# Kernel tuning notes

Measured on AMD Instinct MI355X. Metric: run time of the kernel, lower is better.

Reference implementation:

```python
import jax, jax.numpy as jnp
import numpy as np

N = 100000   # nodes
P = 3        # metapaths
E = 800000   # edges per metapath (avg degree 8)
IN = 128     # in_size
H = 4        # layer_num_heads
D = 32       # out_size per head
HID = 64     # semantic attention hidden
NEG_SLOPE = 0.2


def setup_inputs() -> dict:
    key = jax.random.key(0)
    ks = jax.random.split(key, 10)
    h = jax.random.normal(ks[0], (N, IN), jnp.float32)
    edge_src = jax.random.randint(ks[1], (P, E), 0, N, dtype=jnp.int32).astype(jnp.int64)
    edge_dst = jax.random.randint(ks[2], (P, E), 0, N, dtype=jnp.int32).astype(jnp.int64)
    W = jax.random.normal(ks[3], (P, IN, H * D), jnp.float32) * 0.05
    attn_l = jax.random.normal(ks[4], (P, H, D), jnp.float32) * 0.05
    attn_r = jax.random.normal(ks[5], (P, H, D), jnp.float32) * 0.05
    bias = jnp.zeros((P, H * D), jnp.float32)
    sa_w1 = jax.random.normal(ks[6], (H * D, HID), jnp.float32) * 0.05
    sa_b1 = jnp.zeros((HID,), jnp.float32)
    sa_w2 = jax.random.normal(ks[7], (HID, 1), jnp.float32) * 0.05
    return {"h": h, "edge_src": edge_src, "edge_dst": edge_dst, "W": W,
            "attn_l": attn_l, "attn_r": attn_r, "bias": bias,
            "sa_w1": sa_w1, "sa_b1": sa_b1, "sa_w2": sa_w2}


def _gat_conv(h, src, dst, Wp, al, ar, bp):
    # DGL GATConv: project, per-edge additive attention, edge softmax over dst, scatter-sum.
    n = h.shape[0]
    feat = (h @ Wp).reshape(n, H, D)              # [N,H,D]
    el = (feat * al).sum(-1)                      # [N,H]
    er = (feat * ar).sum(-1)                      # [N,H]
    e = jax.nn.leaky_relu(el[src] + er[dst], NEG_SLOPE)   # [E,H]
    emax = jax.ops.segment_max(e, dst, num_segments=n)    # [N,H]
    emax = jnp.where(jnp.isfinite(emax), emax, 0.0)       # zero-in-degree guard
    ex = jnp.exp(e - emax[dst])                            # [E,H]
    denom = jax.ops.segment_sum(ex, dst, num_segments=n)   # [N,H]
    alpha = ex / jnp.maximum(denom[dst], 1e-9)              # [E,H]
    msg = alpha[:, :, None] * feat[src]                     # [E,H,D]
    out = jax.ops.segment_sum(msg, dst, num_segments=n)     # [N,H,D]
    return out.reshape(n, H * D) + bp


def reference(h, edge_src, edge_dst, W, attn_l, attn_r, bias, sa_w1, sa_b1, sa_w2):
    embs = []
    for p in range(P):  # small fixed metapath set
        embs.append(_gat_conv(h, edge_src[p], edge_dst[p], W[p], attn_l[p], attn_r[p], bias[p]))
    z = jnp.stack(embs, axis=1)                 # [N,P,H*D]
    # SemanticAttention: MLP score, mean over nodes, softmax over metapaths
    w = (jnp.tanh(z @ sa_w1 + sa_b1) @ sa_w2).mean(0)   # [P,1]
    beta = jax.nn.softmax(w, axis=0)                     # [P,1]
    return (beta[None, :, :] * z).sum(1)                 # [N,H*D]
```

## Files before the change

kernel.cpp:

```cpp
#include <hip/hip_runtime.h>
#include <hip/hip_bf16.h>
#include <math.h>

#define NN 100000
#define NP 3
#define NE 800000
#define NH 4
#define ND 32
#define HD 128
#define NHID 64
#define CAP 48

#define S64 64
#define SLICEW 1568
#define CAPB 13504
#define EPT 16
#define FCHUNK (256 * EPT)

typedef __attribute__((ext_vector_type(8))) short short8;
typedef __attribute__((ext_vector_type(4))) float f32x4;

__device__ __forceinline__ unsigned short f2bf(float f) {
  union { float f; unsigned int u; } v; v.f = f;
  unsigned int r = v.u + 0x7FFFu + ((v.u >> 16) & 1u);
  return (unsigned short)(r >> 16);
}
__device__ __forceinline__ float bf2f(unsigned short u) {
  return __uint_as_float(((unsigned int)u) << 16);
}
__device__ __forceinline__ float tanh_fast(float x) {
  return 1.f - 2.f / (1.f + __expf(2.f * x));
}

__global__ __launch_bounds__(256) void prep_kernel(
    const float* __restrict__ h, const float* __restrict__ W, const float* __restrict__ W1,
    unsigned short* __restrict__ hb, unsigned short* __restrict__ WT,
    unsigned short* __restrict__ W1T, int* __restrict__ bucketCnt, float* __restrict__ s) {
  int i = blockIdx.x * blockDim.x + threadIdx.x;
  if (i < NN * 32) {
    float4 v = ((const float4*)h)[i];
    ushort4 o;
    o.x = f2bf(v.x); o.y = f2bf(v.y); o.z = f2bf(v.z); o.w = f2bf(v.w);
    ((ushort4*)hb)[i] = o;
  }
  if (i < NP * 128 * 128) {
    int p = i >> 14, r = i & 16383, n = r >> 7, k = r & 127;
    WT[i] = f2bf(W[(size_t)p * 16384 + k * 128 + n]);
  }
  if (i < NHID * 128) {
    int n = i >> 7, k = i & 127;
    W1T[i] = f2bf(W1[(size_t)k * NHID + n]);
  }
  if (i < NP * S64) bucketCnt[i] = 0;
  if (i < 4) s[i] = 0.f;
}

__global__ __launch_bounds__(256) void gemm_mfma_kernel(
    const unsigned short* __restrict__ hb, const unsigned short* __restrict__ WT_all,
    const float* __restrict__ al_all, const float* __restrict__ ar_all,
    unsigned short* __restrict__ featb_all, float* __restrict__ el_all,
    float* __restrict__ er_all) {
  __shared__ unsigned short Bs[128 * 128];
  const int p = blockIdx.y;
  const unsigned short* WTp = WT_all + (size_t)p * 16384;
#pragma unroll
  for (int it = 0; it < 8; ++it)
    ((float4*)Bs)[it * 256 + threadIdx.x] = ((const float4*)WTp)[it * 256 + threadIdx.x];
  __syncthreads();

  const int wid = threadIdx.x >> 6, lane = threadIdx.x & 63;
  const int c = lane & 15, q = lane >> 4;
  const int tile = blockIdx.x * 4 + wid;
  const int tc = tile < 6250 ? tile : 6249;

  f32x4 acc[8];
#pragma unroll
  for (int t = 0; t < 8; ++t) acc[t] = (f32x4){0.f, 0.f, 0.f, 0.f};

  const unsigned short* arow = hb + (size_t)(tc * 16 + c) * 128 + q * 8;
#pragma unroll
  for (int kc = 0; kc < 4; ++kc) {
    short8 a = *(const short8*)(arow + kc * 32);
#pragma unroll
    for (int t = 0; t < 8; ++t) {
      short8 b = *(const short8*)(Bs + (size_t)(t * 16 + c) * 128 + kc * 32 + q * 8);
      acc[t] = __builtin_amdgcn_mfma_f32_16x16x32_bf16(a, b, acc[t], 0, 0, 0);
    }
  }
  if (tile >= 6250) return;

  unsigned short* featb = featb_all + (size_t)p * NN * 128;
#pragma unroll
  for (int t = 0; t < 8; ++t)
#pragma unroll
    for (int i = 0; i < 4; ++i)
      featb[(size_t)(tc * 16 + q * 4 + i) * 128 + t * 16 + c] = f2bf(acc[t][i]);

  const float* al = al_all + p * 128;
  const float* ar = ar_all + p * 128;
  float alv[8], arv[8];
#pragma unroll
  for (int t = 0; t < 8; ++t) { alv[t] = al[t * 16 + c]; arv[t] = ar[t * 16 + c]; }
  float elp[4][4], erp[4][4];
#pragma unroll
  for (int i = 0; i < 4; ++i)
#pragma unroll
    for (int hh = 0; hh < 4; ++hh) {
      elp[i][hh] = acc[2 * hh][i] * alv[2 * hh] + acc[2 * hh + 1][i] * alv[2 * hh + 1];
      erp[i][hh] = acc[2 * hh][i] * arv[2 * hh] + acc[2 * hh + 1][i] * arv[2 * hh + 1];
    }
#pragma unroll
  for (int m = 1; m <= 8; m <<= 1)
#pragma unroll
    for (int i = 0; i < 4; ++i)
#pragma unroll
      for (int hh = 0; hh < 4; ++hh) {
        elp[i][hh] += __shfl_xor(elp[i][hh], m);
        erp[i][hh] += __shfl_xor(erp[i][hh], m);
      }
  if (c == 0) {
    float* el = el_all + (size_t)p * NN * 4;
    float* er = er_all + (size_t)p * NN * 4;
#pragma unroll
    for (int i = 0; i < 4; ++i) {
      int row = tc * 16 + q * 4 + i;
      *(float4*)(el + (size_t)row * 4) = make_float4(elp[i][0], elp[i][1], elp[i][2], elp[i][3]);
      *(float4*)(er + (size_t)row * 4) = make_float4(erp[i][0], erp[i][1], erp[i][2], erp[i][3]);
    }
  }
}

__global__ __launch_bounds__(256) void fillA_kernel(
    const int* __restrict__ src_all, const int* __restrict__ dst_all,
    int* __restrict__ bucketCnt, int* __restrict__ pairs) {
  __shared__ int histA[S64];
  __shared__ int baseA[S64];
  const int p = blockIdx.y;
  const int e0 = blockIdx.x * FCHUNK + threadIdx.x;
  const int* dstp = dst_all + (size_t)p * NE;
  const int* srcp = src_all + (size_t)p * NE;
  if (threadIdx.x < S64) histA[threadIdx.x] = 0;
  __syncthreads();
  int dv[EPT], sv[EPT];
#pragma unroll
  for (int k = 0; k < EPT; ++k) {
    int e = e0 + k * 256;
    dv[k] = -1; sv[k] = 0;
    if (e < NE) {
      dv[k] = __builtin_nontemporal_load(dstp + e);
      sv[k] = __builtin_nontemporal_load(srcp + e);
    }
    if (dv[k] >= 0) atomicAdd(&histA[(unsigned)dv[k] / SLICEW], 1);
  }
  __syncthreads();
  if (threadIdx.x < S64) {
    baseA[threadIdx.x] = atomicAdd(&bucketCnt[p * S64 + threadIdx.x], histA[threadIdx.x]);
    histA[threadIdx.x] = 0;
  }
  __syncthreads();
#pragma unroll
  for (int k = 0; k < EPT; ++k) {
    if (dv[k] >= 0) {
      int sl = (unsigned)dv[k] / SLICEW;
      int pos = baseA[sl] + atomicAdd(&histA[sl], 1);
      if (pos < CAPB) {
        int dl = dv[k] - sl * SLICEW;
        pairs[((size_t)p * S64 + sl) * CAPB + pos] = (dl << 17) | sv[k];
      }
    }
  }
}

__global__ __launch_bounds__(1024) void fillB_kernel(
    const int* __restrict__ bucketCnt, const int* __restrict__ pairs,
    int* __restrict__ cnt_all, int* __restrict__ elist_all) {
  __shared__ int hist[SLICEW];
  const int p = blockIdx.y, sl = blockIdx.x;
  for (int i = threadIdx.x; i < SLICEW; i += 1024) hist[i] = 0;
  __syncthreads();
  int total = bucketCnt[p * S64 + sl];
  if (total > CAPB) total = CAPB;
  const int* pr = pairs + ((size_t)p * S64 + sl) * CAPB;
  int* elp = elist_all + (size_t)p * NN * CAP;
  for (int i = threadIdx.x; i < total; i += 1024) {
    int pk = pr[i];
    int src = pk & 0x1FFFF;
    int dl = pk >> 17;
    int pos = atomicAdd(&hist[dl], 1);
    if (pos < CAP) elp[(size_t)(sl * SLICEW + dl) * CAP + pos] = src;
  }
  __syncthreads();
  int* cntp = cnt_all + (size_t)p * NN;
  for (int i = threadIdx.x; i < SLICEW; i += 1024) {
    int n = sl * SLICEW + i;
    if (n < NN) cntp[n] = hist[i];
  }
}

__global__ __launch_bounds__(256) void gather_kernel(
    const unsigned short* __restrict__ featb_all, const float* __restrict__ el_all,
    const float* __restrict__ er_all, const int* __restrict__ cnt_all,
    const int* __restrict__ elist_all, const float* __restrict__ bias_all,
    unsigned short* __restrict__ zb) {
  const int p = blockIdx.y;
  const unsigned short* featb = featb_all + (size_t)p * NN * 128;
  const float* el = el_all + (size_t)p * NN * 4;
  const int* elist = elist_all + (size_t)p * NN * CAP;
  const int wid = threadIdx.x >> 6;
  const int lane = threadIdx.x & 63;
  const int n = blockIdx.x * 4 + wid;
  int deg = cnt_all[(size_t)p * NN + n]; deg = deg > CAP ? CAP : deg;
  float4 ern = *(const float4*)(er_all + (size_t)p * NN * 4 + (size_t)n * 4);

  const int j16 = lane & 15, hgrp = lane >> 4;
  const float ernh = hgrp == 0 ? ern.x : hgrp == 1 ? ern.y : hgrp == 2 ? ern.z : ern.w;
  const int sub = lane >> 4, c16 = lane & 15;
  const int hh = c16 >> 2;

  float acc[8] = {0.f, 0.f, 0.f, 0.f, 0.f, 0.f, 0.f, 0.f};
  float dsum = 0.f;

  for (int b = 0; b < deg; b += 16) {
    int s = 0; float x = 0.f;
    int jj = b + j16;
    if (jj < deg) {
      s = elist[(size_t)n * CAP + jj];
      float ev = el[(size_t)s * 4 + hgrp];
      float e = ev + ernh; e = fmaxf(e, 0.2f * e);
      x = __expf(e);
    }
    int bend = deg - b; bend = bend > 16 ? 16 : bend;
    for (int i = 0; i < bend; i += 8) {
      int j0 = i + sub, j1 = i + 4 + sub;
      int s0 = __shfl(s, j0);
      int s1 = __shfl(s, j1);
      float xv0 = __shfl(x, (hh << 4) | j0);
      float xv1 = __shfl(x, (hh << 4) | j1);
      short8 f0 = *(const short8*)(featb + (size_t)s0 * 128 + c16 * 8);
      short8 f1 = *(const short8*)(featb + (size_t)s1 * 128 + c16 * 8);
      dsum += xv0 + xv1;
#pragma unroll
      for (int k = 0; k < 8; ++k) acc[k] += xv0 * bf2f((unsigned short)f0[k]);
#pragma unroll
      for (int k = 0; k < 8; ++k) acc[k] += xv1 * bf2f((unsigned short)f1[k]);
    }
  }
  dsum += __shfl_xor(dsum, 16); dsum += __shfl_xor(dsum, 32);
#pragma unroll
  for (int k = 0; k < 8; ++k) {
    acc[k] += __shfl_xor(acc[k], 16);
    acc[k] += __shfl_xor(acc[k], 32);
  }
  if (sub == 0) {
    float rd = dsum > 0.f ? 1.f / dsum : 0.f;
    const float* bias = bias_all + p * 128 + c16 * 8;
    float4 b0 = *(const float4*)(bias);
    float4 b1 = *(const float4*)(bias + 4);
    short8 o;
    o[0] = f2bf(acc[0] * rd + b0.x); o[1] = f2bf(acc[1] * rd + b0.y);
    o[2] = f2bf(acc[2] * rd + b0.z); o[3] = f2bf(acc[3] * rd + b0.w);
    o[4] = f2bf(acc[4] * rd + b1.x); o[5] = f2bf(acc[5] * rd + b1.y);
    o[6] = f2bf(acc[6] * rd + b1.z); o[7] = f2bf(acc[7] * rd + b1.w);
    *(short8*)(zb + (size_t)n * (NP * 128) + p * 128 + c16 * 8) = o;
  }
}

__global__ __launch_bounds__(256) void sem_mfma_kernel(
    const unsigned short* __restrict__ zb, const unsigned short* __restrict__ W1T,
    const float* __restrict__ b1, const float* __restrict__ w2,
    float* __restrict__ s) {
  __shared__ float red3[3];
  if (threadIdx.x < 3) red3[threadIdx.x] = 0.f;
  __syncthreads();
  const int wid = threadIdx.x >> 6, lane = threadIdx.x & 63;
  const int tile = blockIdx.x * 4 + wid;
  const bool active = tile < 18750;
  const int tc = active ? tile : 18749;
  const int c = lane & 15, q = lane >> 4;
  f32x4 acc[4];
#pragma unroll
  for (int t = 0; t < 4; ++t) acc[t] = (f32x4){0.f, 0.f, 0.f, 0.f};

  const unsigned short* arow = zb + (size_t)(tc * 16 + c) * 128 + q * 8;
  const unsigned short* brow = W1T + (size_t)c * 128 + q * 8;
#pragma unroll
  for (int kc = 0; kc < 4; ++kc) {
    short8 a = *(const short8*)(arow + kc * 32);
#pragma unroll
    for (int t = 0; t < 4; ++t) {
      short8 b = *(const short8*)(brow + (size_t)t * 16 * 128 + kc * 32);
      acc[t] = __builtin_amdgcn_mfma_f32_16x16x32_bf16(a, b, acc[t], 0, 0, 0);
    }
  }
  float part[4] = {0.f, 0.f, 0.f, 0.f};
#pragma unroll
  for (int t = 0; t < 4; ++t) {
    float bb = b1[t * 16 + c], ww = w2[t * 16 + c];
#pragma unroll
    for (int i = 0; i < 4; ++i) part[i] += tanh_fast(acc[t][i] + bb) * ww;
  }
#pragma unroll
  for (int m = 1; m <= 8; m <<= 1)
#pragma unroll
    for (int i = 0; i < 4; ++i) part[i] += __shfl_xor(part[i], m);
  if (active && c == 0) {
#pragma unroll
    for (int i = 0; i < 4; ++i)
      atomicAdd(&red3[(tc * 16 + q * 4 + i) % 3], part[i]);
  }
  __syncthreads();
  if (threadIdx.x < 3) atomicAdd(&s[threadIdx.x], red3[threadIdx.x]);
}

__global__ __launch_bounds__(256) void final_kernel(
    const unsigned short* __restrict__ zb, const float* __restrict__ s,
    float* __restrict__ out) {
  int i = blockIdx.x * blockDim.x + threadIdx.x;
  if (i >= NN * 16) return;
  float w0 = s[0] * (1.f / NN), w1 = s[1] * (1.f / NN), w2c = s[2] * (1.f / NN);
  float m = fmaxf(w0, fmaxf(w1, w2c));
  float e0 = __expf(w0 - m), e1 = __expf(w1 - m), e2 = __expf(w2c - m);
  float inv = 1.f / (e0 + e1 + e2);
  float b0 = e0 * inv, b1 = e1 * inv, b2 = e2 * inv;
  int n = i >> 4, g = i & 15;
  const unsigned short* zr = zb + (size_t)n * (NP * 128) + g * 8;
  ushort4 u0a = *(const ushort4*)(zr);
  ushort4 u0b = *(const ushort4*)(zr + 4);
  ushort4 u1a = *(const ushort4*)(zr + 128);
  ushort4 u1b = *(const ushort4*)(zr + 132);
  ushort4 u2a = *(const ushort4*)(zr + 256);
  ushort4 u2b = *(const ushort4*)(zr + 260);
  float4 oa, ob;
  oa.x = b0 * bf2f(u0a.x) + b1 * bf2f(u1a.x) + b2 * bf2f(u2a.x);
  oa.y = b0 * bf2f(u0a.y) + b1 * bf2f(u1a.y) + b2 * bf2f(u2a.y);
  oa.z = b0 * bf2f(u0a.z) + b1 * bf2f(u1a.z) + b2 * bf2f(u2a.z);
  oa.w = b0 * bf2f(u0a.w) + b1 * bf2f(u1a.w) + b2 * bf2f(u2a.w);
  ob.x = b0 * bf2f(u0b.x) + b1 * bf2f(u1b.x) + b2 * bf2f(u2b.x);
  ob.y = b0 * bf2f(u0b.y) + b1 * bf2f(u1b.y) + b2 * bf2f(u2b.y);
  ob.z = b0 * bf2f(u0b.z) + b1 * bf2f(u1b.z) + b2 * bf2f(u2b.z);
  ob.w = b0 * bf2f(u0b.w) + b1 * bf2f(u1b.w) + b2 * bf2f(u2b.w);
  float* op = out + (size_t)n * 128 + g * 8;
  *(float4*)op = oa;
  *(float4*)(op + 4) = ob;
}

extern "C" void kernel_launch(void* const* d_in, const int* in_sizes, int n_in,
                              void* d_out, int out_size, void* d_ws, size_t ws_size,
                              hipStream_t stream) {
  const float* h    = (const float*)d_in[0];
  const int*   esrc = (const int*)d_in[1];
  const int*   edst = (const int*)d_in[2];
  const float* W    = (const float*)d_in[3];
  const float* al   = (const float*)d_in[4];
  const float* ar   = (const float*)d_in[5];
  const float* bias = (const float*)d_in[6];
  const float* w1   = (const float*)d_in[7];
  const float* b1   = (const float*)d_in[8];
  const float* w2   = (const float*)d_in[9];
  float* out = (float*)d_out;

  unsigned short* zb    = (unsigned short*)d_ws;
  int* pairs = (int*)d_ws;
  unsigned short* featb = zb + (size_t)38400000;
  unsigned short* WT    = featb + (size_t)38400000;
  unsigned short* W1T   = WT + 49152;
  float* el   = (float*)(W1T + 8192);
  float* er   = el + (size_t)NP * NN * 4;
  float* s    = er + (size_t)NP * NN * 4;
  float* beta = s + 16;
  int* bucketCnt = (int*)(beta + 16);
  int* cnt   = bucketCnt + 256;
  int* elist = cnt + (size_t)NP * NN;
  unsigned short* hb = (unsigned short*)elist;

  prep_kernel<<<(NN * 32 + 255) / 256, 256, 0, stream>>>(h, W, w1, hb, WT, W1T, bucketCnt, s);

  dim3 gemmGrid(NN / 64 + 1, NP);
  gemm_mfma_kernel<<<gemmGrid, 256, 0, stream>>>(hb, WT, al, ar, featb, el, er);

  dim3 fillAGrid((NE + FCHUNK - 1) / FCHUNK, NP);
  fillA_kernel<<<fillAGrid, 256, 0, stream>>>(esrc, edst, bucketCnt, pairs);

  dim3 fillBGrid(S64, NP);
  fillB_kernel<<<fillBGrid, 1024, 0, stream>>>(bucketCnt, pairs, cnt, elist);

  dim3 gatherGrid(NN / 4, NP);
  gather_kernel<<<gatherGrid, 256, 0, stream>>>(featb, el, er, cnt, elist, bias, zb);

  sem_mfma_kernel<<<(18750 + 3) / 4, 256, 0, stream>>>(zb, W1T, b1, w2, s);
  final_kernel<<<(NN * 16 + 255) / 256, 256, 0, stream>>>(zb, s, out);
}
```

Baseline: 461.6 us.

## Fuse edge bucketing into prep and CSR build into a slice-local gather kernel

Edge bucketing no longer runs as a separate fillA launch. It moves into the prep kernel and writes per-block histograms and local offsets into fixed per-chunk regions, so no global atomics are needed. The fillB and gather kernels are merged into one gather2 kernel. Each block owns 256 destination nodes, collects their edges from all chunks with a binary search over a prefix scan, sorts them in LDS, and then runs the same attention aggregation. This removes two launches and the padded per-node edge list round trip through global memory, at the cost of serial scans in LDS and far fewer, heavier gather blocks (391×3 of 512 threads). Edges beyond 2560 per slice are dropped.

```diff
diff --git a/kernel.cpp b/kernel.cpp
--- a/kernel.cpp
+++ b/kernel.cpp
@@ -9,13 +9,14 @@
 #define ND 32
 #define HD 128
 #define NHID 64
-#define CAP 48
-
-#define S64 64
-#define SLICEW 1568
-#define CAPB 13504
+
+#define SLW 256
+#define SBK 512
+#define GB 391
+#define NBLK 196
+#define ECHUNK 4096
 #define EPT 16
-#define FCHUNK (256 * EPT)
+#define EMAX 2560
 
 typedef __attribute__((ext_vector_type(8))) short short8;
 typedef __attribute__((ext_vector_type(4))) float f32x4;
@@ -32,27 +33,81 @@
   return 1.f - 2.f / (1.f + __expf(2.f * x));
 }
 
-__global__ __launch_bounds__(256) void prep_kernel(
+__global__ __launch_bounds__(256) void prep_fill_kernel(
     const float* __restrict__ h, const float* __restrict__ W, const float* __restrict__ W1,
+    const int* __restrict__ src_all, const int* __restrict__ dst_all,
     unsigned short* __restrict__ hb, unsigned short* __restrict__ WT,
-    unsigned short* __restrict__ W1T, int* __restrict__ bucketCnt, float* __restrict__ s) {
-  int i = blockIdx.x * blockDim.x + threadIdx.x;
-  if (i < NN * 32) {
-    float4 v = ((const float4*)h)[i];
-    ushort4 o;
-    o.x = f2bf(v.x); o.y = f2bf(v.y); o.z = f2bf(v.z); o.w = f2bf(v.w);
-    ((ushort4*)hb)[i] = o;
-  }
-  if (i < NP * 128 * 128) {
-    int p = i >> 14, r = i & 16383, n = r >> 7, k = r & 127;
-    WT[i] = f2bf(W[(size_t)p * 16384 + k * 128 + n]);
-  }
-  if (i < NHID * 128) {
-    int n = i >> 7, k = i & 127;
-    W1T[i] = f2bf(W1[(size_t)k * NHID + n]);
-  }
-  if (i < NP * S64) bucketCnt[i] = 0;
-  if (i < 4) s[i] = 0.f;
+    unsigned short* __restrict__ W1T, float* __restrict__ s,
+    int* __restrict__ cntA, int* __restrict__ baseA, int* __restrict__ pairs) {
+  __shared__ int hist[SBK];
+  __shared__ int scanb[SBK];
+  const int tid = threadIdx.x;
+  const int bx = blockIdx.x;
+  if (bx < 12500) {
+    int i = bx * 256 + tid;
+    if (i < NN * 32) {
+      float4 v = ((const float4*)h)[i];
+      ushort4 o;
+      o.x = f2bf(v.x); o.y = f2bf(v.y); o.z = f2bf(v.z); o.w = f2bf(v.w);
+      ((ushort4*)hb)[i] = o;
+    }
+    if (i < NP * 128 * 128) {
+      int p = i >> 14, r = i & 16383, n = r >> 7, k = r & 127;
+      WT[i] = f2bf(W[(size_t)p * 16384 + k * 128 + n]);
+    }
+    if (i < NHID * 128) {
+      int n = i >> 7, k = i & 127;
+      W1T[i] = f2bf(W1[(size_t)k * NHID + n]);
+    }
+    if (i < 4) s[i] = 0.f;
+    return;
+  }
+  const int b2 = bx - 12500;
+  const int p = b2 / NBLK, blk = b2 % NBLK;
+  const int* dstp = dst_all + (size_t)p * NE;
+  const int* srcp = src_all + (size_t)p * NE;
+  hist[tid] = 0; hist[tid + 256] = 0;
+  __syncthreads();
+  int dv[EPT], sv[EPT];
+#pragma unroll
+  for (int k = 0; k < EPT; ++k) {
+    int e = blk * ECHUNK + k * 256 + tid;
+    dv[k] = -1; sv[k] = 0;
+    if (e < NE) {
+      dv[k] = __builtin_nontemporal_load(dstp + e);
+      sv[k] = __builtin_nontemporal_load(srcp + e);
+    }
+    if (dv[k] >= 0) atomicAdd(&hist[(unsigned)dv[k] >> 8], 1);
+  }
+  __syncthreads();
+  scanb[tid] = hist[tid]; scanb[tid + 256] = hist[tid + 256];
+  __syncthreads();
+  for (int off = 1; off < SBK; off <<= 1) {
+    int a0 = (tid >= off) ? scanb[tid - off] : 0;
+    int a1 = scanb[tid + 256 - off];
+    __syncthreads();
+    scanb[tid] += a0; scanb[tid + 256] += a1;
+    __syncthreads();
+  }
+  int c0 = hist[tid], c1 = hist[tid + 256];
+  int b0 = scanb[tid] - c0, b1 = scanb[tid + 256] - c1;
+  int* cA = cntA + ((size_t)p * NBLK + blk) * SBK;
+  int* bA = baseA + ((size_t)p * NBLK + blk) * SBK;
+  cA[tid] = c0; cA[tid + 256] = c1;
+  bA[tid] = b0; bA[tid + 256] = b1;
+  __syncthreads();
+  scanb[tid] = b0; scanb[tid + 256] = b1;
+  hist[tid] = 0; hist[tid + 256] = 0;
+  __syncthreads();
+  int* prp = pairs + (size_t)p * NE + (size_t)blk * ECHUNK;
+#pragma unroll
+  for (int k = 0; k < EPT; ++k) {
+    if (dv[k] >= 0) {
+      int sl = (unsigned)dv[k] >> 8;
+      int pos = scanb[sl] + atomicAdd(&hist[sl], 1);
+      prp[pos] = ((dv[k] & 255) << 17) | sv[k];
+    }
+  }
 }
 
 __global__ __launch_bounds__(256) void gemm_mfma_kernel(
@@ -130,138 +185,127 @@
   }
 }
 
-__global__ __launch_bounds__(256) void fillA_kernel(
-    const int* __restrict__ src_all, const int* __restrict__ dst_all,
-    int* __restrict__ bucketCnt, int* __restrict__ pairs) {
-  __shared__ int histA[S64];
-  __shared__ int baseA[S64];
-  const int p = blockIdx.y;
-  const int e0 = blockIdx.x * FCHUNK + threadIdx.x;
-  const int* dstp = dst_all + (size_t)p * NE;
-  const int* srcp = src_all + (size_t)p * NE;
-  if (threadIdx.x < S64) histA[threadIdx.x] = 0;
-  __syncthreads();
-  int dv[EPT], sv[EPT];
-#pragma unroll
-  for (int k = 0; k < EPT; ++k) {
-    int e = e0 + k * 256;
-    dv[k] = -1; sv[k] = 0;
-    if (e < NE) {
-      dv[k] = __builtin_nontemporal_load(dstp + e);
-      sv[k] = __builtin_nontemporal_load(srcp + e);
-    }
-    if (dv[k] >= 0) atomicAdd(&histA[(unsigned)dv[k] / SLICEW], 1);
-  }
-  __syncthreads();
-  if (threadIdx.x < S64) {
-    baseA[threadIdx.x] = atomicAdd(&bucketCnt[p * S64 + threadIdx.x], histA[threadIdx.x]);
-    histA[threadIdx.x] = 0;
-  }
-  __syncthreads();
-#pragma unroll
-  for (int k = 0; k < EPT; ++k) {
-    if (dv[k] >= 0) {
-      int sl = (unsigned)dv[k] / SLICEW;
-      int pos = baseA[sl] + atomicAdd(&histA[sl], 1);
-      if (pos < CAPB) {
-        int dl = dv[k] - sl * SLICEW;
-        pairs[((size_t)p * S64 + sl) * CAPB + pos] = (dl << 17) | sv[k];
-      }
-    }
-  }
-}
-
-__global__ __launch_bounds__(1024) void fillB_kernel(
-    const int* __restrict__ bucketCnt, const int* __restrict__ pairs,
-    int* __restrict__ cnt_all, int* __restrict__ elist_all) {
-  __shared__ int hist[SLICEW];
+__global__ __launch_bounds__(512) void gather2_kernel(
+    const unsigned short* __restrict__ featb_all, const float* __restrict__ el_all,
+    const float* __restrict__ er_all, const int* __restrict__ cntA,
+    const int* __restrict__ baseA, const int* __restrict__ pairs,
+    const float* __restrict__ bias_all, unsigned short* __restrict__ zb) {
+  __shared__ int scnt[NBLK];
+  __shared__ int sbase[NBLK];
+  __shared__ int scum[NBLK];
+  __shared__ int totE;
+  __shared__ int hist[SLW];
+  __shared__ int start[SLW];
+  __shared__ int wcur[SLW];
+  __shared__ int earr[EMAX];
+  __shared__ int srt[EMAX];
+  const int tid = threadIdx.x;
   const int p = blockIdx.y, sl = blockIdx.x;
-  for (int i = threadIdx.x; i < SLICEW; i += 1024) hist[i] = 0;
-  __syncthreads();
-  int total = bucketCnt[p * S64 + sl];
-  if (total > CAPB) total = CAPB;
-  const int* pr = pairs + ((size_t)p * S64 + sl) * CAPB;
-  int* elp = elist_all + (size_t)p * NN * CAP;
-  for (int i = threadIdx.x; i < total; i += 1024) {
-    int pk = pr[i];
-    int src = pk & 0x1FFFF;
-    int dl = pk >> 17;
-    int pos = atomicAdd(&hist[dl], 1);
-    if (pos < CAP) elp[(size_t)(sl * SLICEW + dl) * CAP + pos] = src;
-  }
-  __syncthreads();
-  int* cntp = cnt_all + (size_t)p * NN;
-  for (int i = threadIdx.x; i < SLICEW; i += 1024) {
-    int n = sl * SLICEW + i;
-    if (n < NN) cntp[n] = hist[i];
-  }
-}
-
-__global__ __launch_bounds__(256) void gather_kernel(
-    const unsigned short* __restrict__ featb_all, const float* __restrict__ el_all,
-    const float* __restrict__ er_all, const int* __restrict__ cnt_all,
-    const int* __restrict__ elist_all, const float* __restrict__ bias_all,
-    unsigned short* __restrict__ zb) {
-  const int p = blockIdx.y;
+
+  for (int b = tid; b < NBLK; b += 512) {
+    scnt[b] = cntA[((size_t)p * NBLK + b) * SBK + sl];
+    sbase[b] = baseA[((size_t)p * NBLK + b) * SBK + sl];
+  }
+  if (tid < SLW) hist[tid] = 0;
+  __syncthreads();
+  if (tid < NBLK) scum[tid] = scnt[tid];
+  __syncthreads();
+  for (int off = 1; off < NBLK; off <<= 1) {
+    int a = (tid < NBLK && tid >= off) ? scum[tid - off] : 0;
+    __syncthreads();
+    if (tid < NBLK) scum[tid] += a;
+    __syncthreads();
+  }
+  if (tid == NBLK - 1) { int t = scum[NBLK - 1]; totE = t > EMAX ? EMAX : t; }
+  int excl = (tid < NBLK) ? scum[tid] - scnt[tid] : 0;
+  __syncthreads();
+  if (tid < NBLK) scum[tid] = excl;
+  __syncthreads();
+  const int total = totE;
+  const int* prp = pairs + (size_t)p * NE;
+  for (int e = tid; e < total; e += 512) {
+    int lo = 0, hi = NBLK - 1;
+    while (lo < hi) { int mid = (lo + hi + 1) >> 1; if (scum[mid] <= e) lo = mid; else hi = mid - 1; }
+    int pk = prp[(size_t)lo * ECHUNK + sbase[lo] + (e - scum[lo])];
+    earr[e] = pk;
+    atomicAdd(&hist[pk >> 17], 1);
+  }
+  __syncthreads();
+  if (tid < SLW) start[tid] = hist[tid];
+  __syncthreads();
+  for (int off = 1; off < SLW; off <<= 1) {
+    int a = (tid < SLW && tid >= off) ? start[tid - off] : 0;
+    __syncthreads();
+    if (tid < SLW) start[tid] += a;
+    __syncthreads();
+  }
+  if (tid < SLW) { int st = start[tid] - hist[tid]; start[tid] = st; wcur[tid] = st; }
+  __syncthreads();
+  for (int e = tid; e < total; e += 512) {
+    int pk = earr[e];
+    int pos = atomicAdd(&wcur[pk >> 17], 1);
+    srt[pos] = pk & 0x1FFFF;
+  }
+  __syncthreads();
+
   const unsigned short* featb = featb_all + (size_t)p * NN * 128;
   const float* el = el_all + (size_t)p * NN * 4;
-  const int* elist = elist_all + (size_t)p * NN * CAP;
-  const int wid = threadIdx.x >> 6;
-  const int lane = threadIdx.x & 63;
-  const int n = blockIdx.x * 4 + wid;
-  int deg = cnt_all[(size_t)p * NN + n]; deg = deg > CAP ? CAP : deg;
-  float4 ern = *(const float4*)(er_all + (size_t)p * NN * 4 + (size_t)n * 4);
-
+  const int w = tid >> 6, lane = tid & 63;
   const int j16 = lane & 15, hgrp = lane >> 4;
-  const float ernh = hgrp == 0 ? ern.x : hgrp == 1 ? ern.y : hgrp == 2 ? ern.z : ern.w;
   const int sub = lane >> 4, c16 = lane & 15;
   const int hh = c16 >> 2;
-
-  float acc[8] = {0.f, 0.f, 0.f, 0.f, 0.f, 0.f, 0.f, 0.f};
-  float dsum = 0.f;
-
-  for (int b = 0; b < deg; b += 16) {
-    int s = 0; float x = 0.f;
-    int jj = b + j16;
-    if (jj < deg) {
-      s = elist[(size_t)n * CAP + jj];
-      float ev = el[(size_t)s * 4 + hgrp];
-      float e = ev + ernh; e = fmaxf(e, 0.2f * e);
-      x = __expf(e);
-    }
-    int bend = deg - b; bend = bend > 16 ? 16 : bend;
-    for (int i = 0; i < bend; i += 8) {
-      int j0 = i + sub, j1 = i + 4 + sub;
-      int s0 = __shfl(s, j0);
-      int s1 = __shfl(s, j1);
-      float xv0 = __shfl(x, (hh << 4) | j0);
-      float xv1 = __shfl(x, (hh << 4) | j1);
-      short8 f0 = *(const short8*)(featb + (size_t)s0 * 128 + c16 * 8);
-      short8 f1 = *(const short8*)(featb + (size_t)s1 * 128 + c16 * 8);
-      dsum += xv0 + xv1;
-#pragma unroll
-      for (int k = 0; k < 8; ++k) acc[k] += xv0 * bf2f((unsigned short)f0[k]);
-#pragma unroll
-      for (int k = 0; k < 8; ++k) acc[k] += xv1 * bf2f((unsigned short)f1[k]);
-    }
-  }
-  dsum += __shfl_xor(dsum, 16); dsum += __shfl_xor(dsum, 32);
-#pragma unroll
-  for (int k = 0; k < 8; ++k) {
-    acc[k] += __shfl_xor(acc[k], 16);
-    acc[k] += __shfl_xor(acc[k], 32);
-  }
-  if (sub == 0) {
-    float rd = dsum > 0.f ? 1.f / dsum : 0.f;
-    const float* bias = bias_all + p * 128 + c16 * 8;
-    float4 b0 = *(const float4*)(bias);
-    float4 b1 = *(const float4*)(bias + 4);
-    short8 o;
-    o[0] = f2bf(acc[0] * rd + b0.x); o[1] = f2bf(acc[1] * rd + b0.y);
-    o[2] = f2bf(acc[2] * rd + b0.z); o[3] = f2bf(acc[3] * rd + b0.w);
-    o[4] = f2bf(acc[4] * rd + b1.x); o[5] = f2bf(acc[5] * rd + b1.y);
-    o[6] = f2bf(acc[6] * rd + b1.z); o[7] = f2bf(acc[7] * rd + b1.w);
-    *(short8*)(zb + (size_t)n * (NP * 128) + p * 128 + c16 * 8) = o;
+  for (int nl = w; nl < SLW; nl += 8) {
+    int n = sl * SLW + nl;
+    if (n >= NN) continue;
+    int deg = hist[nl];
+    int st = start[nl];
+    float4 ern = *(const float4*)(er_all + (size_t)p * NN * 4 + (size_t)n * 4);
+    const float ernh = hgrp == 0 ? ern.x : hgrp == 1 ? ern.y : hgrp == 2 ? ern.z : ern.w;
+    float acc[8] = {0.f, 0.f, 0.f, 0.f, 0.f, 0.f, 0.f, 0.f};
+    float dsum = 0.f;
+    for (int b = 0; b < deg; b += 16) {
+      int s = 0; float x = 0.f;
+      int jj = b + j16;
+      if (jj < deg) {
+        s = srt[st + jj];
+        float ev = el[(size_t)s * 4 + hgrp];
+        float e = ev + ernh; e = fmaxf(e, 0.2f * e);
+        x = __expf(e);
+      }
+      int bend = deg - b; bend = bend > 16 ? 16 : bend;
+      for (int i = 0; i < bend; i += 8) {
+        int j0 = i + sub, j1 = i + 4 + sub;
+        int s0 = __shfl(s, j0);
+        int s1 = __shfl(s, j1);
+        float xv0 = __shfl(x, (hh << 4) | j0);
+        float xv1 = __shfl(x, (hh << 4) | j1);
+        short8 f0 = *(const short8*)(featb + (size_t)s0 * 128 + c16 * 8);
+        short8 f1 = *(const short8*)(featb + (size_t)s1 * 128 + c16 * 8);
+        dsum += xv0 + xv1;
+#pragma unroll
+        for (int k = 0; k < 8; ++k) acc[k] += xv0 * bf2f((unsigned short)f0[k]);
+#pragma unroll
+        for (int k = 0; k < 8; ++k) acc[k] += xv1 * bf2f((unsigned short)f1[k]);
+      }
+    }
+    dsum += __shfl_xor(dsum, 16); dsum += __shfl_xor(dsum, 32);
+#pragma unroll
+    for (int k = 0; k < 8; ++k) {
+      acc[k] += __shfl_xor(acc[k], 16);
+      acc[k] += __shfl_xor(acc[k], 32);
+    }
+    if (sub == 0) {
+      float rd = dsum > 0.f ? 1.f / dsum : 0.f;
+      const float* bias = bias_all + p * 128 + c16 * 8;
+      float4 b0 = *(const float4*)(bias);
+      float4 b1 = *(const float4*)(bias + 4);
+      short8 o;
+      o[0] = f2bf(acc[0] * rd + b0.x); o[1] = f2bf(acc[1] * rd + b0.y);
+      o[2] = f2bf(acc[2] * rd + b0.z); o[3] = f2bf(acc[3] * rd + b0.w);
+      o[4] = f2bf(acc[4] * rd + b1.x); o[5] = f2bf(acc[5] * rd + b1.y);
+      o[6] = f2bf(acc[6] * rd + b1.z); o[7] = f2bf(acc[7] * rd + b1.w);
+      *(short8*)(zb + (size_t)n * (NP * 128) + p * 128 + c16 * 8) = o;
+    }
   }
 }
 
@@ -360,32 +404,25 @@
   float* out = (float*)d_out;
 
   unsigned short* zb    = (unsigned short*)d_ws;
-  int* pairs = (int*)d_ws;
   unsigned short* featb = zb + (size_t)38400000;
   unsigned short* WT    = featb + (size_t)38400000;
   unsigned short* W1T   = WT + 49152;
   float* el   = (float*)(W1T + 8192);
   float* er   = el + (size_t)NP * NN * 4;
   float* s    = er + (size_t)NP * NN * 4;
-  float* beta = s + 16;
-  int* bucketCnt = (int*)(beta + 16);
-  int* cnt   = bucketCnt + 256;
-  int* elist = cnt + (size_t)NP * NN;
-  unsigned short* hb = (unsigned short*)elist;
-
-  prep_kernel<<<(NN * 32 + 255) / 256, 256, 0, stream>>>(h, W, w1, hb, WT, W1T, bucketCnt, s);
+  int* cntA  = (int*)(s + 16);
+  int* baseA = cntA + (size_t)NP * NBLK * SBK;
+  int* pairs = baseA + (size_t)NP * NBLK * SBK;
+  unsigned short* hb = (unsigned short*)(pairs + (size_t)NP * NE);
+
+  prep_fill_kernel<<<12500 + NP * NBLK, 256, 0, stream>>>(
+      h, W, w1, esrc, edst, hb, WT, W1T, s, cntA, baseA, pairs);
 
   dim3 gemmGrid(NN / 64 + 1, NP);
   gemm_mfma_kernel<<<gemmGrid, 256, 0, stream>>>(hb, WT, al, ar, featb, el, er);
 
-  dim3 fillAGrid((NE + FCHUNK - 1) / FCHUNK, NP);
-  fillA_kernel<<<fillAGrid, 256, 0, stream>>>(esrc, edst, bucketCnt, pairs);
-
-  dim3 fillBGrid(S64, NP);
-  fillB_kernel<<<fillBGrid, 1024, 0, stream>>>(bucketCnt, pairs, cnt, elist);
-
-  dim3 gatherGrid(NN / 4, NP);
-  gather_kernel<<<gatherGrid, 256, 0, stream>>>(featb, el, er, cnt, elist, bias, zb);
+  dim3 g2Grid(GB, NP);
+  gather2_kernel<<<g2Grid, 512, 0, stream>>>(featb, el, er, cntA, baseA, pairs, bias, zb);
 
   sem_mfma_kernel<<<(18750 + 3) / 4, 256, 0, stream>>>(zb, W1T, b1, w2, s);
   final_kernel<<<(NN * 16 + 255) / 256, 256, 0, stream>>>(zb, s, out);
```

Result: slower. 474.7 us (+2.8%).
